# Performance work log

Measured on AMD Instinct MI355X. Metric: run time of the kernel, lower is better.

The kernel has to match this reference:

```python
import jax, jax.numpy as jnp
import numpy as np

B, S, N, D, H, C = 64, 4, 4096, 1024, 16, 14
HD = D // H
EPS = 1e-5


def _ln(x, g, b):
    m = jnp.mean(x, axis=-1, keepdims=True)
    v = jnp.mean((x - m) ** 2, axis=-1, keepdims=True)
    return (x - m) * jax.lax.rsqrt(v + EPS) * g + b


def setup_inputs() -> dict:
    key = jax.random.key(0)
    ks = jax.random.split(key, 12)
    std = 0.02
    return {
        "cls_tok": jax.random.normal(ks[0], (B, D), jnp.float32),
        "storage": jax.random.normal(ks[1], (B, S, D), jnp.float32),
        "patches": jax.random.normal(ks[2], (B, N, D), jnp.float32),
        "query": jax.random.normal(ks[3], (1, 1, D), jnp.float32) * std,
        "ln_kv_g": jnp.ones((D,), jnp.float32),
        "ln_kv_b": jnp.zeros((D,), jnp.float32),
        "Wq": jax.random.normal(ks[4], (D, D), jnp.float32) / np.sqrt(D).astype(np.float32),
        "Wk": jax.random.normal(ks[5], (D, D), jnp.float32) / np.sqrt(D).astype(np.float32),
        "Wv": jax.random.normal(ks[6], (D, D), jnp.float32) / np.sqrt(D).astype(np.float32),
        "bq": jnp.zeros((D,), jnp.float32),
        "bk": jnp.zeros((D,), jnp.float32),
        "bv": jnp.zeros((D,), jnp.float32),
        "Wo": jax.random.normal(ks[7], (D, D), jnp.float32) / np.sqrt(D).astype(np.float32),
        "bo": jnp.zeros((D,), jnp.float32),
        "ln_out_g": jnp.ones((D,), jnp.float32),
        "ln_out_b": jnp.zeros((D,), jnp.float32),
        "Wp": jax.random.normal(ks[8], (C, D), jnp.float32) * std,
        "bp": jnp.zeros((C,), jnp.float32),
    }


def reference(cls_tok, storage, patches, query, ln_kv_g, ln_kv_b,
              Wq, Wk, Wv, bq, bk, bv, Wo, bo, ln_out_g, ln_out_b, Wp, bp):
    # tokens: (B, L, D) with L = 1 + S + N
    tokens = jnp.concatenate([cls_tok[:, None, :], storage, patches], axis=1)
    kv = _ln(tokens, ln_kv_g, ln_kv_b)
    b = tokens.shape[0]
    q = jnp.broadcast_to(query, (b, 1, D))
    # torch MultiheadAttention: separate q/k/v projections then scaled dot-product
    qp = (q @ Wq.T + bq).reshape(b, 1, H, HD)
    kp = (kv @ Wk.T + bk).reshape(b, -1, H, HD)
    vp = (kv @ Wv.T + bv).reshape(b, -1, H, HD)
    scale = 1.0 / np.sqrt(HD).astype(np.float32)
    scores = jnp.einsum('bqhd,bkhd->bhqk', qp, kp) * scale  # (B, H, 1, L)
    attn = jax.nn.softmax(scores, axis=-1)
    ctx = jnp.einsum('bhqk,bkhd->bqhd', attn, vp).reshape(b, 1, D)
    pooled = ctx[:, 0] @ Wo.T + bo          # out projection, (B, D)
    pooled = _ln(pooled, ln_out_g, ln_out_b)
    return pooled @ Wp.T + bp               # (B, num_labels)
```

## Files before the change

### kernel.cpp

```cpp
#include <hip/hip_runtime.h>
#include <hip/hip_bf16.h>

#define BB 64
#define DD 1024
#define HH 16
#define LL 4101
#define NCH 8
#define CHUNK 513
#define SCALE 0.125f
#define LN_EPS 1e-5f
#define RGS 4104

typedef float  f32x4 __attribute__((ext_vector_type(4)));
typedef short  s16x8 __attribute__((ext_vector_type(8)));
typedef unsigned int u32x4 __attribute__((ext_vector_type(4)));

#define WS_QVEC 0
#define WS_GU   1024
#define WS_G    17408
#define WS_BU   17424
#define WS_CB   17440
#define WS_PL   17456
#define WS_PM   25648
#define WS_PA   33840
#define WS_CTX  8422448
#define WS_POOL 8487984

__device__ __forceinline__ unsigned int pk2(float a, float b) {
    __hip_bfloat162 h = __float22bfloat162_rn(make_float2(a, b));
    unsigned int r;
    __builtin_memcpy(&r, &h, 4);
    return r;
}

__device__ __forceinline__ const float* rowptr(int gr, int b, const float* cls,
                                               const float* sto, const float* pat) {
    if (gr == 0) return cls + (size_t)b * DD;
    if (gr <= 4) return sto + ((size_t)b * 4 + (gr - 1)) * DD;
    return pat + ((size_t)b * 4096 + (gr - 5)) * DD;
}

__global__ void k_qvec(const float* __restrict__ query, const float* __restrict__ Wq,
                       const float* __restrict__ bq, float* __restrict__ qvec) {
    int j = blockIdx.x; int lane = threadIdx.x;
    const float4* wr = reinterpret_cast<const float4*>(Wq + (size_t)j * DD);
    const float4* qr = reinterpret_cast<const float4*>(query);
    float s = 0.f;
#pragma unroll
    for (int k = 0; k < 4; ++k) {
        float4 a = wr[k * 64 + lane];
        float4 q = qr[k * 64 + lane];
        s += a.x * q.x + a.y * q.y + a.z * q.z + a.w * q.w;
    }
#pragma unroll
    for (int m = 1; m < 64; m <<= 1) s += __shfl_xor(s, m, 64);
    if (lane == 0) qvec[j] = s + bq[j];
}

__global__ void k_u(const float* __restrict__ Wk, const float* __restrict__ qvec,
                    const float* __restrict__ g, const float* __restrict__ bln,
                    float* __restrict__ gu, float* __restrict__ Gv, float* __restrict__ Bu) {
    int h = blockIdx.x; int tid = threadIdx.x;
    int w = tid >> 6, lane = tid & 63;
    __shared__ float qs[64];
    __shared__ float red[8];
    if (tid < 64) qs[tid] = qvec[h * 64 + tid];
    __syncthreads();
    int d0 = tid * 4;
    float ax = 0.f, ay = 0.f, az = 0.f, aw = 0.f;
    for (int i = 0; i < 64; ++i) {
        float q = qs[i];
        float4 wv = *reinterpret_cast<const float4*>(&Wk[(size_t)(h * 64 + i) * DD + d0]);
        ax += q * wv.x; ay += q * wv.y; az += q * wv.z; aw += q * wv.w;
    }
    float4 g4 = *reinterpret_cast<const float4*>(&g[d0]);
    float4 b4 = *reinterpret_cast<const float4*>(&bln[d0]);
    float ux = ax * SCALE, uy = ay * SCALE, uz = az * SCALE, uw = aw * SCALE;
    float4 gu4 = make_float4(ux * g4.x, uy * g4.y, uz * g4.z, uw * g4.w);
    *reinterpret_cast<float4*>(&gu[(size_t)h * DD + d0]) = gu4;
    float Gp = gu4.x + gu4.y + gu4.z + gu4.w;
    float Bp = ux * b4.x + uy * b4.y + uz * b4.z + uw * b4.w;
#pragma unroll
    for (int m = 1; m < 64; m <<= 1) { Gp += __shfl_xor(Gp, m, 64); Bp += __shfl_xor(Bp, m, 64); }
    if (lane == 0) { red[2 * w] = Gp; red[2 * w + 1] = Bp; }
    __syncthreads();
    if (tid == 0) {
        Gv[h] = red[0] + red[2] + red[4] + red[6];
        Bu[h] = red[1] + red[3] + red[5] + red[7];
    }
}

__global__ void k_cq(const float* __restrict__ qvec, const float* __restrict__ bk,
                     const float* __restrict__ Bu, float* __restrict__ CB) {
    int h = threadIdx.x;
    if (h < HH) {
        float s = 0.f;
        for (int i = 0; i < 64; ++i) s += qvec[h * 64 + i] * bk[h * 64 + i];
        CB[h] = Bu[h] + s * SCALE;
    }
}

__global__ __launch_bounds__(512, 4) void k_main(
    const float* __restrict__ cls, const float* __restrict__ sto,
    const float* __restrict__ pat, const float* __restrict__ gu,
    const float* __restrict__ Gv, const float* __restrict__ CBv,
    float* __restrict__ pA, float* __restrict__ pl, float* __restrict__ pM) {

    __shared__ __align__(16) ushort Xlds[8 * RGS];
    __shared__ __align__(16) f32x4 csr[8][64];
    __shared__ __align__(16) ushort alds[512];
    __shared__ float2 mrs[32];

    const int blk = blockIdx.x;
    const int b = blk >> 3, ch = blk & 7;
    const int row0 = ch * CHUNK;
    const int rows = min(CHUNK, LL - row0);
    const int nt = (rows + 31) >> 5;
    const int tid = threadIdx.x;
    const int w = tid >> 6, lane = tid & 63;
    const int lm = lane & 15, lg = lane >> 4;
    const int g = w >> 2, wk = w & 3;

    s16x8 guf[8];
    {
        const float* gubase = gu + (size_t)lm * DD + wk * 256 + lg * 8;
#pragma unroll
        for (int s = 0; s < 8; ++s) {
            const float* p = gubase + s * 32;
            u32x4 t;
#pragma unroll
            for (int j = 0; j < 4; ++j) t[j] = pk2(p[2 * j], p[2 * j + 1]);
            guf[s] = __builtin_bit_cast(s16x8, t);
        }
    }
    const float Gh = Gv[lm], CBh = CBv[lm];

    f32x4 acc[8];
#pragma unroll
    for (int i = 0; i < 8; ++i) acc[i] = (f32x4){0.f, 0.f, 0.f, 0.f};
    float lacc = 0.f, macc = 0.f;

    const int C0   = (g * 4 + (lm >> 2)) * RGS + wk * 1024 + (lg >> 1) * 64 + (lm & 3) * 16 + (lg & 1) * 8;
    const int bb4  = lg * 2 * RGS + w * 512 + lm;
    const int aoff = lm * 32 + lg * 8;

    for (int t = 0; t < nt; ++t) {
#pragma unroll
        for (int rr = 0; rr < 4; ++rr) {
            int rl = w * 4 + rr;
            int rloc = t * 32 + rl;
            bool valid = rloc < rows;
            float4 v[4];
#pragma unroll
            for (int it = 0; it < 4; ++it) v[it] = make_float4(0.f, 0.f, 0.f, 0.f);
            if (valid) {
                const float4* s4 = reinterpret_cast<const float4*>(
                    rowptr(row0 + rloc, b, cls, sto, pat));
#pragma unroll
                for (int it = 0; it < 4; ++it) v[it] = s4[it * 64 + lane];
            }
            float s1 = 0.f, s2 = 0.f;
#pragma unroll
            for (int it = 0; it < 4; ++it) {
                float4 q = v[it];
                s1 += q.x + q.y + q.z + q.w;
                s2 += q.x * q.x + q.y * q.y + q.z * q.z + q.w * q.w;
                uint2 pk;
                pk.x = pk2(q.x, q.y);
                pk.y = pk2(q.z, q.w);
                int d0 = 4 * (it * 64 + lane);
                int elem = (rl >> 2) * RGS + (d0 >> 4) * 64 + (rl & 3) * 16 + (d0 & 15);
                *reinterpret_cast<uint2*>(&Xlds[elem]) = pk;
            }
#pragma unroll
            for (int m = 1; m < 64; m <<= 1) {
                s1 += __shfl_xor(s1, m, 64);
                s2 += __shfl_xor(s2, m, 64);
            }
            if (lane == 0) {
                float mean = s1 * (1.f / 1024.f);
                float var = s2 * (1.f / 1024.f) - mean * mean;
                float rstd = rsqrtf(var + LN_EPS);
                mrs[rl] = make_float2(rstd, -mean * rstd);
            }
        }
        __syncthreads();

        {
            f32x4 c0 = {0.f, 0.f, 0.f, 0.f};
#pragma unroll
            for (int s = 0; s < 8; ++s) {
                s16x8 a0 = *reinterpret_cast<const s16x8*>(&Xlds[C0 + s * 128]);
                c0 = __builtin_amdgcn_mfma_f32_16x16x32_bf16(a0, guf[s], c0, 0, 0, 0);
            }
            csr[w][lane] = c0;
        }
        __syncthreads();

        {
#pragma unroll
            for (int gg = 0; gg < 2; ++gg) {
                f32x4 dv = csr[gg * 4][lane];
#pragma unroll
                for (int wp = 1; wp < 4; ++wp) dv += csr[gg * 4 + wp][lane];
                int rbase = gg * 16 + lg * 4;
                float al[4];
#pragma unroll
                for (int i = 0; i < 4; ++i) {
                    float2 mr = mrs[rbase + i];
                    float sc = dv[i] * mr.x + (mr.y * Gh + CBh);
                    bool vld = (t * 32 + rbase + i) < rows;
                    float p = vld ? __expf(sc) : 0.f;
                    lacc += p;
                    macc += p * mr.y;
                    al[i] = p * mr.x;
                }
                *reinterpret_cast<unsigned int*>(&alds[lm * 32 + rbase])     = pk2(al[0], al[1]);
                *reinterpret_cast<unsigned int*>(&alds[lm * 32 + rbase + 2]) = pk2(al[2], al[3]);
            }
        }
        asm volatile("s_waitcnt lgkmcnt(0)" ::: "memory");
        __builtin_amdgcn_sched_barrier(0);

        {
            s16x8 af = *reinterpret_cast<const s16x8*>(&alds[aoff]);
#pragma unroll
            for (int dt = 0; dt < 8; ++dt) {
                s16x8 bfrag;
#pragma unroll
                for (int j = 0; j < 8; ++j) {
                    int e = bb4 + dt * 64 + ((j & 3) << 4) + (j >> 2) * RGS;
                    bfrag[j] = (short)Xlds[e];
                }
                acc[dt] = __builtin_amdgcn_mfma_f32_16x16x32_bf16(af, bfrag, acc[dt], 0, 0, 0);
            }
        }
        __syncthreads();
    }

    size_t pabase = ((size_t)blk << 14);
#pragma unroll
    for (int dt = 0; dt < 8; ++dt) {
#pragma unroll
        for (int i = 0; i < 4; ++i) {
            int h = lg * 4 + i;
            pA[pabase + ((size_t)h << 10) + w * 128 + dt * 16 + lm] = acc[dt][i];
        }
    }
    if (w == 0) {
        lacc += __shfl_xor(lacc, 16, 64); lacc += __shfl_xor(lacc, 32, 64);
        macc += __shfl_xor(macc, 16, 64); macc += __shfl_xor(macc, 32, 64);
        if (lane < 16) {
            pl[blk * 16 + lane] = lacc;
            pM[blk * 16 + lane] = -macc;
        }
    }
}

__global__ void k_comb(float* __restrict__ pA, const float* __restrict__ pl,
                       const float* __restrict__ pM, const float* __restrict__ g,
                       const float* __restrict__ bln) {
    int blk = blockIdx.x; int b = blk >> 4; int h = blk & 15; int tid = threadIdx.x;
    float l = 0.f, M = 0.f;
#pragma unroll
    for (int ch = 0; ch < NCH; ++ch) {
        l += pl[(b * NCH + ch) * 16 + h];
        M += pM[(b * NCH + ch) * 16 + h];
    }
    float inv = 1.f / l;
    float4 s = make_float4(0.f, 0.f, 0.f, 0.f);
#pragma unroll
    for (int ch = 0; ch < NCH; ++ch) {
        const float4* p4 = reinterpret_cast<const float4*>(
            pA + (((size_t)(b * NCH + ch) * 16 + h) << 10));
        float4 v = p4[tid];
        s.x += v.x; s.y += v.y; s.z += v.z; s.w += v.w;
    }
    float4 g4 = *reinterpret_cast<const float4*>(&g[tid * 4]);
    float4 b4 = *reinterpret_cast<const float4*>(&bln[tid * 4]);
    float4 o;
    o.x = g4.x * (s.x - M) * inv + b4.x;
    o.y = g4.y * (s.y - M) * inv + b4.y;
    o.z = g4.z * (s.z - M) * inv + b4.z;
    o.w = g4.w * (s.w - M) * inv + b4.w;
    float4* dst = reinterpret_cast<float4*>(pA + (((size_t)(b * NCH) * 16 + h) << 10));
    dst[tid] = o;
}

__global__ void k_ctx(const float* __restrict__ Wv, const float* __restrict__ bv,
                      const float* __restrict__ pA, float* __restrict__ ctx) {
    int j = blockIdx.x; int h = j >> 6;
    int w = threadIdx.x >> 6, lane = threadIdx.x & 63;
    const float4* wr = reinterpret_cast<const float4*>(Wv + (size_t)j * DD);
    float4 wv[4];
#pragma unroll
    for (int k = 0; k < 4; ++k) wv[k] = wr[k * 64 + lane];
    float bvj = bv[j];
    for (int bb2 = w * 16; bb2 < w * 16 + 16; ++bb2) {
        const float4* sr = reinterpret_cast<const float4*>(
            pA + (((size_t)(bb2 * NCH) * 16 + h) << 10));
        float s = 0.f;
#pragma unroll
        for (int k = 0; k < 4; ++k) {
            float4 v = sr[k * 64 + lane];
            s += wv[k].x * v.x + wv[k].y * v.y + wv[k].z * v.z + wv[k].w * v.w;
        }
#pragma unroll
        for (int m = 1; m < 64; m <<= 1) s += __shfl_xor(s, m, 64);
        if (lane == 0) ctx[(size_t)bb2 * DD + j] = s + bvj;
    }
}

__global__ void k_pool(const float* __restrict__ Wo, const float* __restrict__ bo,
                       const float* __restrict__ ctx, float* __restrict__ pooled) {
    int j = blockIdx.x;
    int w = threadIdx.x >> 6, lane = threadIdx.x & 63;
    const float4* wr = reinterpret_cast<const float4*>(Wo + (size_t)j * DD);
    float4 wv[4];
#pragma unroll
    for (int k = 0; k < 4; ++k) wv[k] = wr[k * 64 + lane];
    float boj = bo[j];
    for (int bb2 = w * 16; bb2 < w * 16 + 16; ++bb2) {
        const float4* cr4 = reinterpret_cast<const float4*>(ctx + (size_t)bb2 * DD);
        float s = 0.f;
#pragma unroll
        for (int k = 0; k < 4; ++k) {
            float4 v = cr4[k * 64 + lane];
            s += wv[k].x * v.x + wv[k].y * v.y + wv[k].z * v.z + wv[k].w * v.w;
        }
#pragma unroll
        for (int m = 1; m < 64; m <<= 1) s += __shfl_xor(s, m, 64);
        if (lane == 0) pooled[(size_t)bb2 * DD + j] = s + boj;
    }
}

__global__ void k_head(const float* __restrict__ pooled, const float* __restrict__ g2,
                       const float* __restrict__ b2, const float* __restrict__ Wp,
                       const float* __restrict__ bp, float* __restrict__ out) {
    int b = blockIdx.x; int tid = threadIdx.x;
    __shared__ float pln[DD];
    __shared__ float red[8];
    const float4* pr = reinterpret_cast<const float4*>(pooled + (size_t)b * DD);
    float4 v = pr[tid];
    float s1 = v.x + v.y + v.z + v.w;
    float s2 = v.x * v.x + v.y * v.y + v.z * v.z + v.w * v.w;
#pragma unroll
    for (int m = 1; m < 64; m <<= 1) { s1 += __shfl_xor(s1, m, 64); s2 += __shfl_xor(s2, m, 64); }
    int w = tid >> 6, lane = tid & 63;
    if (lane == 0) { red[2 * w] = s1; red[2 * w + 1] = s2; }
    __syncthreads();
    s1 = red[0] + red[2] + red[4] + red[6];
    s2 = red[1] + red[3] + red[5] + red[7];
    float mean = s1 * (1.f / 1024.f);
    float var  = s2 * (1.f / 1024.f) - mean * mean;
    float rstd = rsqrtf(var + LN_EPS);
    int d0 = tid * 4;
    pln[d0 + 0] = (v.x - mean) * rstd * g2[d0 + 0] + b2[d0 + 0];
    pln[d0 + 1] = (v.y - mean) * rstd * g2[d0 + 1] + b2[d0 + 1];
    pln[d0 + 2] = (v.z - mean) * rstd * g2[d0 + 2] + b2[d0 + 2];
    pln[d0 + 3] = (v.w - mean) * rstd * g2[d0 + 3] + b2[d0 + 3];
    __syncthreads();
    int q = tid & 15, c = tid >> 4;
    if (c < 14) {
        float s = 0.f;
#pragma unroll 8
        for (int i = 0; i < 64; ++i) {
            int d = i * 16 + q;
            s += pln[d] * Wp[c * DD + d];
        }
#pragma unroll
        for (int m = 1; m < 16; m <<= 1) s += __shfl_xor(s, m, 64);
        if (q == 0) out[b * 14 + c] = s + bp[c];
    }
}

extern "C" void kernel_launch(void* const* d_in, const int* in_sizes, int n_in,
                              void* d_out, int out_size, void* d_ws, size_t ws_size,
                              hipStream_t stream) {
    const float* cls   = (const float*)d_in[0];
    const float* sto   = (const float*)d_in[1];
    const float* pat   = (const float*)d_in[2];
    const float* query = (const float*)d_in[3];
    const float* g     = (const float*)d_in[4];
    const float* bln   = (const float*)d_in[5];
    const float* Wq    = (const float*)d_in[6];
    const float* Wk    = (const float*)d_in[7];
    const float* Wv    = (const float*)d_in[8];
    const float* bq    = (const float*)d_in[9];
    const float* bk    = (const float*)d_in[10];
    const float* bv    = (const float*)d_in[11];
    const float* Wo    = (const float*)d_in[12];
    const float* bo    = (const float*)d_in[13];
    const float* g2    = (const float*)d_in[14];
    const float* b2    = (const float*)d_in[15];
    const float* Wp    = (const float*)d_in[16];
    const float* bp    = (const float*)d_in[17];

    float* ws     = (float*)d_ws;
    float* qvec   = ws + WS_QVEC;
    float* gu     = ws + WS_GU;
    float* Gv     = ws + WS_G;
    float* Bu     = ws + WS_BU;
    float* CB     = ws + WS_CB;
    float* pl     = ws + WS_PL;
    float* pM     = ws + WS_PM;
    float* pA     = ws + WS_PA;
    float* ctx    = ws + WS_CTX;
    float* pooled = ws + WS_POOL;
    float* out    = (float*)d_out;

    hipLaunchKernelGGL(k_qvec, dim3(1024), dim3(64), 0, stream, query, Wq, bq, qvec);
    hipLaunchKernelGGL(k_u,    dim3(16),   dim3(256), 0, stream, Wk, qvec, g, bln, gu, Gv, Bu);
    hipLaunchKernelGGL(k_cq,   dim3(1),    dim3(64), 0, stream, qvec, bk, Bu, CB);
    hipLaunchKernelGGL(k_main, dim3(BB * NCH), dim3(512), 0, stream,
                       cls, sto, pat, gu, Gv, CB, pA, pl, pM);
    hipLaunchKernelGGL(k_comb, dim3(BB * HH), dim3(256), 0, stream, pA, pl, pM, g, bln);
    hipLaunchKernelGGL(k_ctx,  dim3(1024), dim3(256), 0, stream, Wv, bv, pA, ctx);
    hipLaunchKernelGGL(k_pool, dim3(1024), dim3(256), 0, stream, Wo, bo, ctx, pooled);
    hipLaunchKernelGGL(k_head, dim3(64),   dim3(256), 0, stream, pooled, g2, b2, Wp, bp, out);
}
```

Before: 287.3 us.

## Double-buffer 16-row LDS tiles and prefetch next rows into registers

Shrinks the per-iteration tile from 32 to 16 rows and keeps two LDS buffers in a simple row-major layout with padded row stride. The next tile's global rows are prefetched into registers while the current tile is processed, and the score MFMA reduction is split across all 8 waves. The value-accumulation MFMA runs once per pair of tiles, drawing its K=32 operand from both buffers. It also swaps __syncthreads for explicit waitcnt plus s_barrier. The aim is to hide global load latency behind compute and cut LDS footprint for occupancy, at the cost of more loop iterations and barriers, plus extra register pressure from the prefetch buffer.

```diff
diff --git a/kernel.cpp b/kernel.cpp
--- a/kernel.cpp
+++ b/kernel.cpp
@@ -9,7 +9,8 @@
 #define CHUNK 513
 #define SCALE 0.125f
 #define LN_EPS 1e-5f
-#define RGS 4104
+#define XROW 1032
+#define XBUF (16 * XROW)
 
 typedef float  f32x4 __attribute__((ext_vector_type(4)));
 typedef short  s16x8 __attribute__((ext_vector_type(8)));
@@ -106,26 +107,25 @@
     const float* __restrict__ Gv, const float* __restrict__ CBv,
     float* __restrict__ pA, float* __restrict__ pl, float* __restrict__ pM) {
 
-    __shared__ __align__(16) ushort Xlds[8 * RGS];
+    __shared__ __align__(16) ushort Xb[2 * XBUF];
     __shared__ __align__(16) f32x4 csr[8][64];
-    __shared__ __align__(16) ushort alds[512];
-    __shared__ float2 mrs[32];
+    __shared__ __align__(16) ushort alds[16 * 32];
+    __shared__ float2 mrs[16];
 
     const int blk = blockIdx.x;
     const int b = blk >> 3, ch = blk & 7;
     const int row0 = ch * CHUNK;
     const int rows = min(CHUNK, LL - row0);
-    const int nt = (rows + 31) >> 5;
+    const int nt = (rows + 15) >> 4;
     const int tid = threadIdx.x;
     const int w = tid >> 6, lane = tid & 63;
     const int lm = lane & 15, lg = lane >> 4;
-    const int g = w >> 2, wk = w & 3;
-
-    s16x8 guf[8];
+
+    s16x8 guf[4];
     {
-        const float* gubase = gu + (size_t)lm * DD + wk * 256 + lg * 8;
-#pragma unroll
-        for (int s = 0; s < 8; ++s) {
+        const float* gubase = gu + (size_t)lm * DD + w * 128 + lg * 8;
+#pragma unroll
+        for (int s = 0; s < 4; ++s) {
             const float* p = gubase + s * 32;
             u32x4 t;
 #pragma unroll
@@ -140,37 +140,39 @@
     for (int i = 0; i < 8; ++i) acc[i] = (f32x4){0.f, 0.f, 0.f, 0.f};
     float lacc = 0.f, macc = 0.f;
 
-    const int C0   = (g * 4 + (lm >> 2)) * RGS + wk * 1024 + (lg >> 1) * 64 + (lm & 3) * 16 + (lg & 1) * 8;
-    const int bb4  = lg * 2 * RGS + w * 512 + lm;
+    const int C0   = lm * XROW + w * 128 + lg * 8;
     const int aoff = lm * 32 + lg * 8;
 
+    float4 pf[2][4];
+#pragma unroll
+    for (int rr = 0; rr < 2; ++rr) {
+#pragma unroll
+        for (int it = 0; it < 4; ++it) pf[rr][it] = make_float4(0.f, 0.f, 0.f, 0.f);
+        int rloc = 2 * w + rr;
+        if (rloc < rows) {
+            const float4* s4 = reinterpret_cast<const float4*>(
+                rowptr(row0 + rloc, b, cls, sto, pat));
+#pragma unroll
+            for (int it = 0; it < 4; ++it) pf[rr][it] = s4[it * 64 + lane];
+        }
+    }
+
+    int cur = 0;
     for (int t = 0; t < nt; ++t) {
 #pragma unroll
-        for (int rr = 0; rr < 4; ++rr) {
-            int rl = w * 4 + rr;
-            int rloc = t * 32 + rl;
-            bool valid = rloc < rows;
-            float4 v[4];
-#pragma unroll
-            for (int it = 0; it < 4; ++it) v[it] = make_float4(0.f, 0.f, 0.f, 0.f);
-            if (valid) {
-                const float4* s4 = reinterpret_cast<const float4*>(
-                    rowptr(row0 + rloc, b, cls, sto, pat));
-#pragma unroll
-                for (int it = 0; it < 4; ++it) v[it] = s4[it * 64 + lane];
-            }
+        for (int rr = 0; rr < 2; ++rr) {
+            int rl = 2 * w + rr;
             float s1 = 0.f, s2 = 0.f;
 #pragma unroll
             for (int it = 0; it < 4; ++it) {
-                float4 q = v[it];
+                float4 q = pf[rr][it];
                 s1 += q.x + q.y + q.z + q.w;
                 s2 += q.x * q.x + q.y * q.y + q.z * q.z + q.w * q.w;
                 uint2 pk;
                 pk.x = pk2(q.x, q.y);
                 pk.y = pk2(q.z, q.w);
-                int d0 = 4 * (it * 64 + lane);
-                int elem = (rl >> 2) * RGS + (d0 >> 4) * 64 + (rl & 3) * 16 + (d0 & 15);
-                *reinterpret_cast<uint2*>(&Xlds[elem]) = pk;
+                int e = cur * XBUF + rl * XROW + it * 256 + lane * 4;
+                *reinterpret_cast<uint2*>(&Xb[e]) = pk;
             }
 #pragma unroll
             for (int m = 1; m < 64; m <<= 1) {
@@ -184,58 +186,80 @@
                 mrs[rl] = make_float2(rstd, -mean * rstd);
             }
         }
-        __syncthreads();
+#pragma unroll
+        for (int rr = 0; rr < 2; ++rr) {
+#pragma unroll
+            for (int it = 0; it < 4; ++it) pf[rr][it] = make_float4(0.f, 0.f, 0.f, 0.f);
+            int rloc = (t + 1) * 16 + 2 * w + rr;
+            if (t + 1 < nt && rloc < rows) {
+                const float4* s4 = reinterpret_cast<const float4*>(
+                    rowptr(row0 + rloc, b, cls, sto, pat));
+#pragma unroll
+                for (int it = 0; it < 4; ++it) pf[rr][it] = s4[it * 64 + lane];
+            }
+        }
+        asm volatile("s_waitcnt lgkmcnt(0)" ::: "memory");
+        __builtin_amdgcn_s_barrier();
 
         {
             f32x4 c0 = {0.f, 0.f, 0.f, 0.f};
 #pragma unroll
-            for (int s = 0; s < 8; ++s) {
-                s16x8 a0 = *reinterpret_cast<const s16x8*>(&Xlds[C0 + s * 128]);
+            for (int s = 0; s < 4; ++s) {
+                s16x8 a0 = *reinterpret_cast<const s16x8*>(&Xb[cur * XBUF + C0 + s * 32]);
                 c0 = __builtin_amdgcn_mfma_f32_16x16x32_bf16(a0, guf[s], c0, 0, 0, 0);
             }
             csr[w][lane] = c0;
         }
-        __syncthreads();
+        asm volatile("s_waitcnt lgkmcnt(0)" ::: "memory");
+        __builtin_amdgcn_s_barrier();
 
         {
-#pragma unroll
-            for (int gg = 0; gg < 2; ++gg) {
-                f32x4 dv = csr[gg * 4][lane];
-#pragma unroll
-                for (int wp = 1; wp < 4; ++wp) dv += csr[gg * 4 + wp][lane];
-                int rbase = gg * 16 + lg * 4;
-                float al[4];
-#pragma unroll
-                for (int i = 0; i < 4; ++i) {
-                    float2 mr = mrs[rbase + i];
-                    float sc = dv[i] * mr.x + (mr.y * Gh + CBh);
-                    bool vld = (t * 32 + rbase + i) < rows;
-                    float p = vld ? __expf(sc) : 0.f;
-                    lacc += p;
-                    macc += p * mr.y;
-                    al[i] = p * mr.x;
-                }
-                *reinterpret_cast<unsigned int*>(&alds[lm * 32 + rbase])     = pk2(al[0], al[1]);
-                *reinterpret_cast<unsigned int*>(&alds[lm * 32 + rbase + 2]) = pk2(al[2], al[3]);
+            f32x4 dv = csr[0][lane];
+#pragma unroll
+            for (int wp = 1; wp < 8; ++wp) dv += csr[wp][lane];
+            int rbase = lg * 4;
+            int p16 = (t & 1) * 16;
+            float al[4];
+#pragma unroll
+            for (int i = 0; i < 4; ++i) {
+                float2 mr = mrs[rbase + i];
+                float sc = dv[i] * mr.x + (mr.y * Gh + CBh);
+                bool vld = (t * 16 + rbase + i) < rows;
+                float p = vld ? __expf(sc) : 0.f;
+                lacc += p;
+                macc += p * mr.y;
+                al[i] = p * mr.x;
+            }
+            *reinterpret_cast<unsigned int*>(&alds[lm * 32 + p16 + rbase])     = pk2(al[0], al[1]);
+            *reinterpret_cast<unsigned int*>(&alds[lm * 32 + p16 + rbase + 2]) = pk2(al[2], al[3]);
+            if ((t == nt - 1) && !(t & 1)) {
+                *reinterpret_cast<unsigned int*>(&alds[lm * 32 + 16 + rbase])     = 0u;
+                *reinterpret_cast<unsigned int*>(&alds[lm * 32 + 16 + rbase + 2]) = 0u;
             }
         }
         asm volatile("s_waitcnt lgkmcnt(0)" ::: "memory");
         __builtin_amdgcn_sched_barrier(0);
 
-        {
+        if ((t & 1) || (t == nt - 1)) {
+            int bufA = (t & 1) ? (cur ^ 1) : cur;
+            int bufB = cur;
+            int myBuf = (lg >= 2) ? bufB : bufA;
+            int rbase16 = (lg * 8) & 15;
+            const ushort* xb = &Xb[myBuf * XBUF + rbase16 * XROW + w * 128 + lm];
             s16x8 af = *reinterpret_cast<const s16x8*>(&alds[aoff]);
 #pragma unroll
             for (int dt = 0; dt < 8; ++dt) {
                 s16x8 bfrag;
 #pragma unroll
                 for (int j = 0; j < 8; ++j) {
-                    int e = bb4 + dt * 64 + ((j & 3) << 4) + (j >> 2) * RGS;
-                    bfrag[j] = (short)Xlds[e];
+                    bfrag[j] = (short)xb[dt * 16 + j * XROW];
                 }
                 acc[dt] = __builtin_amdgcn_mfma_f32_16x16x32_bf16(af, bfrag, acc[dt], 0, 0, 0);
             }
         }
-        __syncthreads();
+        asm volatile("s_waitcnt lgkmcnt(0)" ::: "memory");
+        __builtin_amdgcn_s_barrier();
+        cur ^= 1;
     }
 
     size_t pabase = ((size_t)blk << 14);
```

Result: slower. 353.6 us (+23.1%).

## Double-buffer row tiles via async global-to-LDS loads and MFMA-based LN stats

Applied to the files above, without the earlier changes.

The main kernel now streams 16-row fp32 tiles straight into a double-buffered LDS region with global_load_lds, so the next tile's loads overlap compute on the current one. Per-row LayerNorm sums are computed with extra MFMAs (x·x and x·ones) instead of shuffle reductions, and the chunk count drops from 8 to 4 per batch with one block per CU. The u-vector precompute is also split across 4x more blocks, with partial sums combined in k_cq. This trades grid parallelism (256 blocks) and bf16 conversion done during LDS reads for overlapped memory traffic.

```diff
diff --git a/kernel.cpp b/kernel.cpp
--- a/kernel.cpp
+++ b/kernel.cpp
@@ -5,11 +5,12 @@
 #define DD 1024
 #define HH 16
 #define LL 4101
-#define NCH 8
-#define CHUNK 513
+#define NCH 4
+#define CHUNK 1026
 #define SCALE 0.125f
 #define LN_EPS 1e-5f
-#define RGS 4104
+#define XROWF 1028
+#define BUFF  (16 * XROWF)
 
 typedef float  f32x4 __attribute__((ext_vector_type(4)));
 typedef short  s16x8 __attribute__((ext_vector_type(8)));
@@ -18,13 +19,14 @@
 #define WS_QVEC 0
 #define WS_GU   1024
 #define WS_G    17408
-#define WS_BU   17424
-#define WS_CB   17440
-#define WS_PL   17456
-#define WS_PM   25648
-#define WS_PA   33840
-#define WS_CTX  8422448
-#define WS_POOL 8487984
+#define WS_CB   17424
+#define WS_GP   17440
+#define WS_BP   17504
+#define WS_PL   17568
+#define WS_PM   21664
+#define WS_PA   25760
+#define WS_CTX  4220064
+#define WS_POOL 4285600
 
 __device__ __forceinline__ unsigned int pk2(float a, float b) {
     __hip_bfloat162 h = __float22bfloat162_rn(make_float2(a, b));
@@ -59,80 +61,86 @@
 
 __global__ void k_u(const float* __restrict__ Wk, const float* __restrict__ qvec,
                     const float* __restrict__ g, const float* __restrict__ bln,
-                    float* __restrict__ gu, float* __restrict__ Gv, float* __restrict__ Bu) {
-    int h = blockIdx.x; int tid = threadIdx.x;
+                    float* __restrict__ gu, float* __restrict__ Gp, float* __restrict__ Bp) {
+    int h = blockIdx.x >> 2, q = blockIdx.x & 3;
+    int tid = threadIdx.x;
     int w = tid >> 6, lane = tid & 63;
     __shared__ float qs[64];
     __shared__ float red[8];
     if (tid < 64) qs[tid] = qvec[h * 64 + tid];
     __syncthreads();
-    int d0 = tid * 4;
-    float ax = 0.f, ay = 0.f, az = 0.f, aw = 0.f;
-    for (int i = 0; i < 64; ++i) {
-        float q = qs[i];
-        float4 wv = *reinterpret_cast<const float4*>(&Wk[(size_t)(h * 64 + i) * DD + d0]);
-        ax += q * wv.x; ay += q * wv.y; az += q * wv.z; aw += q * wv.w;
-    }
-    float4 g4 = *reinterpret_cast<const float4*>(&g[d0]);
-    float4 b4 = *reinterpret_cast<const float4*>(&bln[d0]);
-    float ux = ax * SCALE, uy = ay * SCALE, uz = az * SCALE, uw = aw * SCALE;
-    float4 gu4 = make_float4(ux * g4.x, uy * g4.y, uz * g4.z, uw * g4.w);
-    *reinterpret_cast<float4*>(&gu[(size_t)h * DD + d0]) = gu4;
-    float Gp = gu4.x + gu4.y + gu4.z + gu4.w;
-    float Bp = ux * b4.x + uy * b4.y + uz * b4.z + uw * b4.w;
-#pragma unroll
-    for (int m = 1; m < 64; m <<= 1) { Gp += __shfl_xor(Gp, m, 64); Bp += __shfl_xor(Bp, m, 64); }
-    if (lane == 0) { red[2 * w] = Gp; red[2 * w + 1] = Bp; }
+    int d = q * 256 + tid;
+    float a = 0.f;
+#pragma unroll 8
+    for (int i = 0; i < 64; ++i) a += qs[i] * Wk[(size_t)(h * 64 + i) * DD + d];
+    float u = a * SCALE;
+    float guv = u * g[d];
+    gu[(size_t)h * DD + d] = guv;
+    float Gv_ = guv, Bv_ = u * bln[d];
+#pragma unroll
+    for (int m = 1; m < 64; m <<= 1) { Gv_ += __shfl_xor(Gv_, m, 64); Bv_ += __shfl_xor(Bv_, m, 64); }
+    if (lane == 0) { red[2 * w] = Gv_; red[2 * w + 1] = Bv_; }
     __syncthreads();
     if (tid == 0) {
-        Gv[h] = red[0] + red[2] + red[4] + red[6];
-        Bu[h] = red[1] + red[3] + red[5] + red[7];
+        Gp[h * 4 + q] = red[0] + red[2] + red[4] + red[6];
+        Bp[h * 4 + q] = red[1] + red[3] + red[5] + red[7];
     }
 }
 
 __global__ void k_cq(const float* __restrict__ qvec, const float* __restrict__ bk,
-                     const float* __restrict__ Bu, float* __restrict__ CB) {
+                     const float* __restrict__ Gp, const float* __restrict__ Bp,
+                     float* __restrict__ Gv, float* __restrict__ CB) {
     int h = threadIdx.x;
     if (h < HH) {
+        float G = Gp[h * 4] + Gp[h * 4 + 1] + Gp[h * 4 + 2] + Gp[h * 4 + 3];
+        float Bu = Bp[h * 4] + Bp[h * 4 + 1] + Bp[h * 4 + 2] + Bp[h * 4 + 3];
         float s = 0.f;
         for (int i = 0; i < 64; ++i) s += qvec[h * 64 + i] * bk[h * 64 + i];
-        CB[h] = Bu[h] + s * SCALE;
-    }
-}
-
-__global__ __launch_bounds__(512, 4) void k_main(
+        Gv[h] = G;
+        CB[h] = Bu + s * SCALE;
+    }
+}
+
+__global__ __launch_bounds__(512, 1) void k_main(
     const float* __restrict__ cls, const float* __restrict__ sto,
     const float* __restrict__ pat, const float* __restrict__ gu,
     const float* __restrict__ Gv, const float* __restrict__ CBv,
     float* __restrict__ pA, float* __restrict__ pl, float* __restrict__ pM) {
 
-    __shared__ __align__(16) ushort Xlds[8 * RGS];
+    __shared__ __align__(16) float Xf[2 * BUFF];
     __shared__ __align__(16) f32x4 csr[8][64];
-    __shared__ __align__(16) ushort alds[512];
-    __shared__ float2 mrs[32];
+    __shared__ float sstat[2][16][8];
+    __shared__ float2 mrs[16];
+    __shared__ __align__(8) ushort alds[16 * 32];
 
     const int blk = blockIdx.x;
-    const int b = blk >> 3, ch = blk & 7;
+    const int b = blk >> 2, ch = blk & 3;
     const int row0 = ch * CHUNK;
     const int rows = min(CHUNK, LL - row0);
-    const int nt = (rows + 31) >> 5;
+    const int nt = (rows + 15) >> 4;
     const int tid = threadIdx.x;
     const int w = tid >> 6, lane = tid & 63;
     const int lm = lane & 15, lg = lane >> 4;
-    const int g = w >> 2, wk = w & 3;
-
-    s16x8 guf[8];
+
+    for (int i = tid; i < 2 * BUFF; i += 512) Xf[i] = 0.f;
+    if (tid < 256) reinterpret_cast<unsigned int*>(alds)[tid] = 0u;
+
+    s16x8 guf[4];
     {
-        const float* gubase = gu + (size_t)lm * DD + wk * 256 + lg * 8;
-#pragma unroll
-        for (int s = 0; s < 8; ++s) {
+        const float* gubase = gu + (size_t)lm * DD + w * 128 + lg * 8;
+#pragma unroll
+        for (int s = 0; s < 4; ++s) {
             const float* p = gubase + s * 32;
             u32x4 t;
 #pragma unroll
             for (int j = 0; j < 4; ++j) t[j] = pk2(p[2 * j], p[2 * j + 1]);
-            guf[s] = __builtin_bit_cast(s16x8, t);
-        }
-    }
+            s16x8 f; __builtin_memcpy(&f, &t, 16);
+            guf[s] = f;
+        }
+    }
+    s16x8 ones;
+#pragma unroll
+    for (int j = 0; j < 8; ++j) ones[j] = (short)0x3F80;
     const float Gh = Gv[lm], CBh = CBv[lm];
 
     f32x4 acc[8];
@@ -140,102 +148,116 @@
     for (int i = 0; i < 8; ++i) acc[i] = (f32x4){0.f, 0.f, 0.f, 0.f};
     float lacc = 0.f, macc = 0.f;
 
-    const int C0   = (g * 4 + (lm >> 2)) * RGS + wk * 1024 + (lg >> 1) * 64 + (lm & 3) * 16 + (lg & 1) * 8;
-    const int bb4  = lg * 2 * RGS + w * 512 + lm;
-    const int aoff = lm * 32 + lg * 8;
+#define ISSUE_TILE(T)                                                              \
+    {                                                                              \
+        int buf_ = (T) & 1;                                                        \
+        _Pragma("unroll")                                                          \
+        for (int rr = 0; rr < 2; ++rr) {                                           \
+            int rl = 2 * w + rr;                                                   \
+            int rloc = (T) * 16 + rl;                                              \
+            if (rloc < rows) {                                                     \
+                const float* rp = rowptr(row0 + rloc, b, cls, sto, pat);           \
+                _Pragma("unroll")                                                  \
+                for (int c = 0; c < 4; ++c) {                                      \
+                    __builtin_amdgcn_global_load_lds(                              \
+                        (const __attribute__((address_space(1))) unsigned int*)    \
+                            (rp + c * 256 + lane * 4),                             \
+                        (__attribute__((address_space(3))) unsigned int*)          \
+                            (&Xf[buf_ * BUFF + rl * XROWF + c * 256]),             \
+                        16, 0, 0);                                                 \
+                }                                                                  \
+            }                                                                      \
+        }                                                                          \
+    }
+
+    __syncthreads();
+    ISSUE_TILE(0);
+    __syncthreads();
 
     for (int t = 0; t < nt; ++t) {
-#pragma unroll
-        for (int rr = 0; rr < 4; ++rr) {
-            int rl = w * 4 + rr;
-            int rloc = t * 32 + rl;
-            bool valid = rloc < rows;
-            float4 v[4];
-#pragma unroll
-            for (int it = 0; it < 4; ++it) v[it] = make_float4(0.f, 0.f, 0.f, 0.f);
-            if (valid) {
-                const float4* s4 = reinterpret_cast<const float4*>(
-                    rowptr(row0 + rloc, b, cls, sto, pat));
-#pragma unroll
-                for (int it = 0; it < 4; ++it) v[it] = s4[it * 64 + lane];
-            }
-            float s1 = 0.f, s2 = 0.f;
-#pragma unroll
-            for (int it = 0; it < 4; ++it) {
-                float4 q = v[it];
-                s1 += q.x + q.y + q.z + q.w;
-                s2 += q.x * q.x + q.y * q.y + q.z * q.z + q.w * q.w;
-                uint2 pk;
-                pk.x = pk2(q.x, q.y);
-                pk.y = pk2(q.z, q.w);
-                int d0 = 4 * (it * 64 + lane);
-                int elem = (rl >> 2) * RGS + (d0 >> 4) * 64 + (rl & 3) * 16 + (d0 & 15);
-                *reinterpret_cast<uint2*>(&Xlds[elem]) = pk;
-            }
-#pragma unroll
-            for (int m = 1; m < 64; m <<= 1) {
-                s1 += __shfl_xor(s1, m, 64);
-                s2 += __shfl_xor(s2, m, 64);
-            }
-            if (lane == 0) {
-                float mean = s1 * (1.f / 1024.f);
-                float var = s2 * (1.f / 1024.f) - mean * mean;
-                float rstd = rsqrtf(var + LN_EPS);
-                mrs[rl] = make_float2(rstd, -mean * rstd);
-            }
-        }
-        __syncthreads();
+        const int buf = t & 1;
+        if (t + 1 < nt) ISSUE_TILE(t + 1);
 
         {
-            f32x4 c0 = {0.f, 0.f, 0.f, 0.f};
-#pragma unroll
-            for (int s = 0; s < 8; ++s) {
-                s16x8 a0 = *reinterpret_cast<const s16x8*>(&Xlds[C0 + s * 128]);
+            f32x4 c0 = {0.f,0.f,0.f,0.f}, q0 = {0.f,0.f,0.f,0.f}, m0 = {0.f,0.f,0.f,0.f};
+            const float* Ab = &Xf[buf * BUFF + lm * XROWF + w * 128 + lg * 8];
+#pragma unroll
+            for (int s = 0; s < 4; ++s) {
+                float4 x0 = *reinterpret_cast<const float4*>(Ab + s * 32);
+                float4 x1 = *reinterpret_cast<const float4*>(Ab + s * 32 + 4);
+                u32x4 tt;
+                tt[0] = pk2(x0.x, x0.y); tt[1] = pk2(x0.z, x0.w);
+                tt[2] = pk2(x1.x, x1.y); tt[3] = pk2(x1.z, x1.w);
+                s16x8 a0; __builtin_memcpy(&a0, &tt, 16);
                 c0 = __builtin_amdgcn_mfma_f32_16x16x32_bf16(a0, guf[s], c0, 0, 0, 0);
+                q0 = __builtin_amdgcn_mfma_f32_16x16x32_bf16(a0, a0,     q0, 0, 0, 0);
+                m0 = __builtin_amdgcn_mfma_f32_16x16x32_bf16(a0, ones,   m0, 0, 0, 0);
             }
             csr[w][lane] = c0;
-        }
-        __syncthreads();
-
-        {
-#pragma unroll
-            for (int gg = 0; gg < 2; ++gg) {
-                f32x4 dv = csr[gg * 4][lane];
-#pragma unroll
-                for (int wp = 1; wp < 4; ++wp) dv += csr[gg * 4 + wp][lane];
-                int rbase = gg * 16 + lg * 4;
-                float al[4];
-#pragma unroll
-                for (int i = 0; i < 4; ++i) {
-                    float2 mr = mrs[rbase + i];
-                    float sc = dv[i] * mr.x + (mr.y * Gh + CBh);
-                    bool vld = (t * 32 + rbase + i) < rows;
-                    float p = vld ? __expf(sc) : 0.f;
-                    lacc += p;
-                    macc += p * mr.y;
-                    al[i] = p * mr.x;
-                }
-                *reinterpret_cast<unsigned int*>(&alds[lm * 32 + rbase])     = pk2(al[0], al[1]);
-                *reinterpret_cast<unsigned int*>(&alds[lm * 32 + rbase + 2]) = pk2(al[2], al[3]);
+            if (lg == (lm >> 2)) sstat[0][lm][w] = q0[lm & 3];
+            if (lm == 0) {
+#pragma unroll
+                for (int i = 0; i < 4; ++i) sstat[1][lg * 4 + i][w] = m0[i];
             }
+        }
+        asm volatile("s_waitcnt lgkmcnt(0)" ::: "memory");
+        __builtin_amdgcn_s_barrier();
+
+        if (lane < 16) {
+            const float4* q4 = reinterpret_cast<const float4*>(&sstat[0][lane][0]);
+            float4 qa = q4[0], qb = q4[1];
+            const float4* m4 = reinterpret_cast<const float4*>(&sstat[1][lane][0]);
+            float4 ma = m4[0], mb = m4[1];
+            float s2 = qa.x + qa.y + qa.z + qa.w + qb.x + qb.y + qb.z + qb.w;
+            float s1 = ma.x + ma.y + ma.z + ma.w + mb.x + mb.y + mb.z + mb.w;
+            float mean = s1 * (1.f / 1024.f);
+            float var  = s2 * (1.f / 1024.f) - mean * mean;
+            float rstd = rsqrtf(var + LN_EPS);
+            mrs[lane] = make_float2(rstd, -mean * rstd);
         }
         asm volatile("s_waitcnt lgkmcnt(0)" ::: "memory");
         __builtin_amdgcn_sched_barrier(0);
-
         {
-            s16x8 af = *reinterpret_cast<const s16x8*>(&alds[aoff]);
+            f32x4 dv = csr[0][lane];
+#pragma unroll
+            for (int wp = 1; wp < 8; ++wp) dv += csr[wp][lane];
+            int rbase = lg * 4;
+            float al[4];
+#pragma unroll
+            for (int i = 0; i < 4; ++i) {
+                float2 mr = mrs[rbase + i];
+                float sc = dv[i] * mr.x + (mr.y * Gh + CBh);
+                bool vld = (t * 16 + rbase + i) < rows;
+                float p = vld ? __expf(sc) : 0.f;
+                lacc += p;
+                macc += p * mr.y;
+                al[i] = p * mr.x;
+            }
+            *reinterpret_cast<unsigned int*>(&alds[lm * 32 + rbase])     = pk2(al[0], al[1]);
+            *reinterpret_cast<unsigned int*>(&alds[lm * 32 + rbase + 2]) = pk2(al[2], al[3]);
+        }
+        asm volatile("s_waitcnt lgkmcnt(0)" ::: "memory");
+        __builtin_amdgcn_sched_barrier(0);
+
+        {
+            s16x8 af = *reinterpret_cast<const s16x8*>(&alds[lm * 32 + lg * 8]);
+            const float* Bb = &Xf[buf * BUFF + (lg & 1) * 8 * XROWF + w * 128 + lm];
+            bool act = lg < 2;
 #pragma unroll
             for (int dt = 0; dt < 8; ++dt) {
-                s16x8 bfrag;
-#pragma unroll
-                for (int j = 0; j < 8; ++j) {
-                    int e = bb4 + dt * 64 + ((j & 3) << 4) + (j >> 2) * RGS;
-                    bfrag[j] = (short)Xlds[e];
-                }
-                acc[dt] = __builtin_amdgcn_mfma_f32_16x16x32_bf16(af, bfrag, acc[dt], 0, 0, 0);
+                float bx[8];
+#pragma unroll
+                for (int j = 0; j < 8; ++j) bx[j] = act ? Bb[j * XROWF + dt * 16] : 0.f;
+                u32x4 tb;
+                tb[0] = pk2(bx[0], bx[1]); tb[1] = pk2(bx[2], bx[3]);
+                tb[2] = pk2(bx[4], bx[5]); tb[3] = pk2(bx[6], bx[7]);
+                s16x8 bf; __builtin_memcpy(&bf, &tb, 16);
+                acc[dt] = __builtin_amdgcn_mfma_f32_16x16x32_bf16(af, bf, acc[dt], 0, 0, 0);
             }
         }
-        __syncthreads();
+        asm volatile("s_waitcnt vmcnt(0)" ::: "memory");
+        asm volatile("s_waitcnt lgkmcnt(0)" ::: "memory");
+        __builtin_amdgcn_s_barrier();
     }
 
     size_t pabase = ((size_t)blk << 14);
@@ -255,6 +277,7 @@
             pM[blk * 16 + lane] = -macc;
         }
     }
+#undef ISSUE_TILE
 }
 
 __global__ void k_comb(float* __restrict__ pA, const float* __restrict__ pl,
@@ -400,8 +423,9 @@
     float* qvec   = ws + WS_QVEC;
     float* gu     = ws + WS_GU;
     float* Gv     = ws + WS_G;
-    float* Bu     = ws + WS_BU;
     float* CB     = ws + WS_CB;
+    float* Gp     = ws + WS_GP;
+    float* Bp     = ws + WS_BP;
     float* pl     = ws + WS_PL;
     float* pM     = ws + WS_PM;
     float* pA     = ws + WS_PA;
@@ -410,8 +434,8 @@
     float* out    = (float*)d_out;
 
     hipLaunchKernelGGL(k_qvec, dim3(1024), dim3(64), 0, stream, query, Wq, bq, qvec);
-    hipLaunchKernelGGL(k_u,    dim3(16),   dim3(256), 0, stream, Wk, qvec, g, bln, gu, Gv, Bu);
-    hipLaunchKernelGGL(k_cq,   dim3(1),    dim3(64), 0, stream, qvec, bk, Bu, CB);
+    hipLaunchKernelGGL(k_u,    dim3(64),   dim3(256), 0, stream, Wk, qvec, g, bln, gu, Gp, Bp);
+    hipLaunchKernelGGL(k_cq,   dim3(1),    dim3(64), 0, stream, qvec, bk, Gp, Bp, Gv, CB);
     hipLaunchKernelGGL(k_main, dim3(BB * NCH), dim3(512), 0, stream,
                        cls, sto, pat, gu, Gv, CB, pA, pl, pM);
     hipLaunchKernelGGL(k_comb, dim3(BB * HH), dim3(256), 0, stream, pA, pl, pM, g, bln);
```

Result: slower. 428.4 us (+49.1%).

## Shrink main attention blocks to 4 waves and split sequence into 12 chunks

Applied to the files above, without the earlier changes.

The main fused LN+score+weighted-sum kernel now uses 256-thread blocks processing 16 rows per tile instead of 512 threads and 32 rows. Each wave owns a full 256-wide slice of the D dimension with 16 accumulators. The sequence is split into 12 chunks when workspace permits, giving more blocks for better occupancy and CU coverage. The k_u precompute is also spread over 64 blocks with partial sums reduced in k_cq. The trade-offs are more partial results to combine, half-idle lanes in the weighted-sum MFMA, and more register pressure from the larger accumulator set.

```diff
diff --git a/kernel.cpp b/kernel.cpp
--- a/kernel.cpp
+++ b/kernel.cpp
@@ -5,11 +5,9 @@
 #define DD 1024
 #define HH 16
 #define LL 4101
-#define NCH 8
-#define CHUNK 513
 #define SCALE 0.125f
 #define LN_EPS 1e-5f
-#define RGS 4104
+#define RGS 4112
 
 typedef float  f32x4 __attribute__((ext_vector_type(4)));
 typedef short  s16x8 __attribute__((ext_vector_type(8)));
@@ -18,13 +16,12 @@
 #define WS_QVEC 0
 #define WS_GU   1024
 #define WS_G    17408
-#define WS_BU   17424
-#define WS_CB   17440
-#define WS_PL   17456
-#define WS_PM   25648
-#define WS_PA   33840
-#define WS_CTX  8422448
-#define WS_POOL 8487984
+#define WS_CB   17424
+#define WS_GP   17440
+#define WS_BP   17504
+#define WS_PL   17568
+#define WS_PM   29856
+#define WS_PA   42144
 
 __device__ __forceinline__ unsigned int pk2(float a, float b) {
     __hip_bfloat162 h = __float22bfloat162_rn(make_float2(a, b));
@@ -59,96 +56,99 @@
 
 __global__ void k_u(const float* __restrict__ Wk, const float* __restrict__ qvec,
                     const float* __restrict__ g, const float* __restrict__ bln,
-                    float* __restrict__ gu, float* __restrict__ Gv, float* __restrict__ Bu) {
-    int h = blockIdx.x; int tid = threadIdx.x;
+                    float* __restrict__ gu, float* __restrict__ Gp, float* __restrict__ Bp) {
+    int h = blockIdx.x >> 2, q = blockIdx.x & 3;
+    int tid = threadIdx.x;
     int w = tid >> 6, lane = tid & 63;
     __shared__ float qs[64];
     __shared__ float red[8];
     if (tid < 64) qs[tid] = qvec[h * 64 + tid];
     __syncthreads();
-    int d0 = tid * 4;
-    float ax = 0.f, ay = 0.f, az = 0.f, aw = 0.f;
-    for (int i = 0; i < 64; ++i) {
-        float q = qs[i];
-        float4 wv = *reinterpret_cast<const float4*>(&Wk[(size_t)(h * 64 + i) * DD + d0]);
-        ax += q * wv.x; ay += q * wv.y; az += q * wv.z; aw += q * wv.w;
-    }
-    float4 g4 = *reinterpret_cast<const float4*>(&g[d0]);
-    float4 b4 = *reinterpret_cast<const float4*>(&bln[d0]);
-    float ux = ax * SCALE, uy = ay * SCALE, uz = az * SCALE, uw = aw * SCALE;
-    float4 gu4 = make_float4(ux * g4.x, uy * g4.y, uz * g4.z, uw * g4.w);
-    *reinterpret_cast<float4*>(&gu[(size_t)h * DD + d0]) = gu4;
-    float Gp = gu4.x + gu4.y + gu4.z + gu4.w;
-    float Bp = ux * b4.x + uy * b4.y + uz * b4.z + uw * b4.w;
-#pragma unroll
-    for (int m = 1; m < 64; m <<= 1) { Gp += __shfl_xor(Gp, m, 64); Bp += __shfl_xor(Bp, m, 64); }
-    if (lane == 0) { red[2 * w] = Gp; red[2 * w + 1] = Bp; }
+    int d = q * 256 + tid;
+    float a = 0.f;
+#pragma unroll 8
+    for (int i = 0; i < 64; ++i) a += qs[i] * Wk[(size_t)(h * 64 + i) * DD + d];
+    float u = a * SCALE;
+    float guv = u * g[d];
+    gu[(size_t)h * DD + d] = guv;
+    float Gv_ = guv, Bv_ = u * bln[d];
+#pragma unroll
+    for (int m = 1; m < 64; m <<= 1) { Gv_ += __shfl_xor(Gv_, m, 64); Bv_ += __shfl_xor(Bv_, m, 64); }
+    if (lane == 0) { red[2 * w] = Gv_; red[2 * w + 1] = Bv_; }
     __syncthreads();
     if (tid == 0) {
-        Gv[h] = red[0] + red[2] + red[4] + red[6];
-        Bu[h] = red[1] + red[3] + red[5] + red[7];
+        Gp[h * 4 + q] = red[0] + red[2] + red[4] + red[6];
+        Bp[h * 4 + q] = red[1] + red[3] + red[5] + red[7];
     }
 }
 
 __global__ void k_cq(const float* __restrict__ qvec, const float* __restrict__ bk,
-                     const float* __restrict__ Bu, float* __restrict__ CB) {
+                     const float* __restrict__ Gp, const float* __restrict__ Bp,
+                     float* __restrict__ Gv, float* __restrict__ CB) {
     int h = threadIdx.x;
     if (h < HH) {
+        float G = Gp[h * 4] + Gp[h * 4 + 1] + Gp[h * 4 + 2] + Gp[h * 4 + 3];
+        float Bu = Bp[h * 4] + Bp[h * 4 + 1] + Bp[h * 4 + 2] + Bp[h * 4 + 3];
         float s = 0.f;
         for (int i = 0; i < 64; ++i) s += qvec[h * 64 + i] * bk[h * 64 + i];
-        CB[h] = Bu[h] + s * SCALE;
-    }
-}
-
-__global__ __launch_bounds__(512, 4) void k_main(
+        Gv[h] = G;
+        CB[h] = Bu + s * SCALE;
+    }
+}
+
+__global__ __launch_bounds__(256, 3) void k_main(
     const float* __restrict__ cls, const float* __restrict__ sto,
     const float* __restrict__ pat, const float* __restrict__ gu,
     const float* __restrict__ Gv, const float* __restrict__ CBv,
-    float* __restrict__ pA, float* __restrict__ pl, float* __restrict__ pM) {
-
-    __shared__ __align__(16) ushort Xlds[8 * RGS];
-    __shared__ __align__(16) f32x4 csr[8][64];
-    __shared__ __align__(16) ushort alds[512];
-    __shared__ float2 mrs[32];
+    float* __restrict__ pA, float* __restrict__ pl, float* __restrict__ pM,
+    int nch, int chunk) {
+
+    __shared__ __align__(16) ushort Xs[4 * RGS];
+    __shared__ __align__(16) f32x4 csr[4][64];
+    __shared__ __align__(8) ushort alds[512];
+    __shared__ float2 mrs[16];
 
     const int blk = blockIdx.x;
-    const int b = blk >> 3, ch = blk & 7;
-    const int row0 = ch * CHUNK;
-    const int rows = min(CHUNK, LL - row0);
-    const int nt = (rows + 31) >> 5;
+    const int b = blk / nch, ch = blk - b * nch;
+    const int row0 = ch * chunk;
+    const int rows = min(chunk, LL - row0);
+    const int nt = (rows + 15) >> 4;
     const int tid = threadIdx.x;
     const int w = tid >> 6, lane = tid & 63;
     const int lm = lane & 15, lg = lane >> 4;
-    const int g = w >> 2, wk = w & 3;
+
+    if (tid < 256) reinterpret_cast<unsigned int*>(alds)[tid] = 0u;
 
     s16x8 guf[8];
     {
-        const float* gubase = gu + (size_t)lm * DD + wk * 256 + lg * 8;
+        const float* gubase = gu + (size_t)lm * DD + w * 256 + lg * 8;
 #pragma unroll
         for (int s = 0; s < 8; ++s) {
             const float* p = gubase + s * 32;
             u32x4 t;
 #pragma unroll
             for (int j = 0; j < 4; ++j) t[j] = pk2(p[2 * j], p[2 * j + 1]);
-            guf[s] = __builtin_bit_cast(s16x8, t);
+            s16x8 f; __builtin_memcpy(&f, &t, 16);
+            guf[s] = f;
         }
     }
     const float Gh = Gv[lm], CBh = CBv[lm];
 
-    f32x4 acc[8];
-#pragma unroll
-    for (int i = 0; i < 8; ++i) acc[i] = (f32x4){0.f, 0.f, 0.f, 0.f};
+    f32x4 acc[16];
+#pragma unroll
+    for (int i = 0; i < 16; ++i) acc[i] = (f32x4){0.f, 0.f, 0.f, 0.f};
     float lacc = 0.f, macc = 0.f;
 
-    const int C0   = (g * 4 + (lm >> 2)) * RGS + wk * 1024 + (lg >> 1) * 64 + (lm & 3) * 16 + (lg & 1) * 8;
-    const int bb4  = lg * 2 * RGS + w * 512 + lm;
-    const int aoff = lm * 32 + lg * 8;
+    const int C0 = (lm >> 2) * RGS + w * 1024 + (lg >> 1) * 64 + (lm & 3) * 16 + (lg & 1) * 8;
+    const bool act = lg < 2;
+
+    __syncthreads();
 
     for (int t = 0; t < nt; ++t) {
-#pragma unroll
+#pragma unroll 2
         for (int rr = 0; rr < 4; ++rr) {
             int rl = w * 4 + rr;
-            int rloc = t * 32 + rl;
+            int rloc = t * 16 + rl;
             bool valid = rloc < rows;
             float4 v[4];
 #pragma unroll
@@ -170,7 +170,7 @@
                 pk.y = pk2(q.z, q.w);
                 int d0 = 4 * (it * 64 + lane);
                 int elem = (rl >> 2) * RGS + (d0 >> 4) * 64 + (rl & 3) * 16 + (d0 & 15);
-                *reinterpret_cast<uint2*>(&Xlds[elem]) = pk;
+                *reinterpret_cast<uint2*>(&Xs[elem]) = pk;
             }
 #pragma unroll
             for (int m = 1; m < 64; m <<= 1) {
@@ -190,7 +190,7 @@
             f32x4 c0 = {0.f, 0.f, 0.f, 0.f};
 #pragma unroll
             for (int s = 0; s < 8; ++s) {
-                s16x8 a0 = *reinterpret_cast<const s16x8*>(&Xlds[C0 + s * 128]);
+                s16x8 a0 = *reinterpret_cast<const s16x8*>(&Xs[C0 + s * 128]);
                 c0 = __builtin_amdgcn_mfma_f32_16x16x32_bf16(a0, guf[s], c0, 0, 0, 0);
             }
             csr[w][lane] = c0;
@@ -198,39 +198,36 @@
         __syncthreads();
 
         {
-#pragma unroll
-            for (int gg = 0; gg < 2; ++gg) {
-                f32x4 dv = csr[gg * 4][lane];
-#pragma unroll
-                for (int wp = 1; wp < 4; ++wp) dv += csr[gg * 4 + wp][lane];
-                int rbase = gg * 16 + lg * 4;
-                float al[4];
-#pragma unroll
-                for (int i = 0; i < 4; ++i) {
-                    float2 mr = mrs[rbase + i];
-                    float sc = dv[i] * mr.x + (mr.y * Gh + CBh);
-                    bool vld = (t * 32 + rbase + i) < rows;
-                    float p = vld ? __expf(sc) : 0.f;
-                    lacc += p;
-                    macc += p * mr.y;
-                    al[i] = p * mr.x;
-                }
-                *reinterpret_cast<unsigned int*>(&alds[lm * 32 + rbase])     = pk2(al[0], al[1]);
-                *reinterpret_cast<unsigned int*>(&alds[lm * 32 + rbase + 2]) = pk2(al[2], al[3]);
-            }
+            f32x4 dv = csr[0][lane];
+#pragma unroll
+            for (int wp = 1; wp < 4; ++wp) dv += csr[wp][lane];
+            int rbase = lg * 4;
+            float al[4];
+#pragma unroll
+            for (int i = 0; i < 4; ++i) {
+                float2 mr = mrs[rbase + i];
+                float sc = dv[i] * mr.x + (mr.y * Gh + CBh);
+                bool vld = (t * 16 + rbase + i) < rows;
+                float p = vld ? __expf(sc) : 0.f;
+                lacc += p;
+                macc += p * mr.y;
+                al[i] = p * mr.x;
+            }
+            *reinterpret_cast<unsigned int*>(&alds[lm * 32 + rbase])     = pk2(al[0], al[1]);
+            *reinterpret_cast<unsigned int*>(&alds[lm * 32 + rbase + 2]) = pk2(al[2], al[3]);
         }
         asm volatile("s_waitcnt lgkmcnt(0)" ::: "memory");
         __builtin_amdgcn_sched_barrier(0);
 
         {
-            s16x8 af = *reinterpret_cast<const s16x8*>(&alds[aoff]);
-#pragma unroll
-            for (int dt = 0; dt < 8; ++dt) {
+            s16x8 af = *reinterpret_cast<const s16x8*>(&alds[lm * 32 + lg * 8]);
+#pragma unroll
+            for (int dt = 0; dt < 16; ++dt) {
                 s16x8 bfrag;
 #pragma unroll
                 for (int j = 0; j < 8; ++j) {
-                    int e = bb4 + dt * 64 + ((j & 3) << 4) + (j >> 2) * RGS;
-                    bfrag[j] = (short)Xlds[e];
+                    int e = (lg * 2 + (j >> 2)) * RGS + (w * 16 + dt) * 64 + (j & 3) * 16 + lm;
+                    bfrag[j] = act ? (short)Xs[e] : (short)0;
                 }
                 acc[dt] = __builtin_amdgcn_mfma_f32_16x16x32_bf16(af, bfrag, acc[dt], 0, 0, 0);
             }
@@ -240,11 +237,11 @@
 
     size_t pabase = ((size_t)blk << 14);
 #pragma unroll
-    for (int dt = 0; dt < 8; ++dt) {
+    for (int dt = 0; dt < 16; ++dt) {
 #pragma unroll
         for (int i = 0; i < 4; ++i) {
             int h = lg * 4 + i;
-            pA[pabase + ((size_t)h << 10) + w * 128 + dt * 16 + lm] = acc[dt][i];
+            pA[pabase + ((size_t)h << 10) + w * 256 + dt * 16 + lm] = acc[dt][i];
         }
     }
     if (w == 0) {
@@ -259,20 +256,18 @@
 
 __global__ void k_comb(float* __restrict__ pA, const float* __restrict__ pl,
                        const float* __restrict__ pM, const float* __restrict__ g,
-                       const float* __restrict__ bln) {
+                       const float* __restrict__ bln, int nch) {
     int blk = blockIdx.x; int b = blk >> 4; int h = blk & 15; int tid = threadIdx.x;
     float l = 0.f, M = 0.f;
-#pragma unroll
-    for (int ch = 0; ch < NCH; ++ch) {
-        l += pl[(b * NCH + ch) * 16 + h];
-        M += pM[(b * NCH + ch) * 16 + h];
+    for (int ch = 0; ch < nch; ++ch) {
+        l += pl[(b * nch + ch) * 16 + h];
+        M += pM[(b * nch + ch) * 16 + h];
     }
     float inv = 1.f / l;
     float4 s = make_float4(0.f, 0.f, 0.f, 0.f);
-#pragma unroll
-    for (int ch = 0; ch < NCH; ++ch) {
+    for (int ch = 0; ch < nch; ++ch) {
         const float4* p4 = reinterpret_cast<const float4*>(
-            pA + (((size_t)(b * NCH + ch) * 16 + h) << 10));
+            pA + (((size_t)(b * nch + ch) * 16 + h) << 10));
         float4 v = p4[tid];
         s.x += v.x; s.y += v.y; s.z += v.z; s.w += v.w;
     }
@@ -283,12 +278,12 @@
     o.y = g4.y * (s.y - M) * inv + b4.y;
     o.z = g4.z * (s.z - M) * inv + b4.z;
     o.w = g4.w * (s.w - M) * inv + b4.w;
-    float4* dst = reinterpret_cast<float4*>(pA + (((size_t)(b * NCH) * 16 + h) << 10));
+    float4* dst = reinterpret_cast<float4*>(pA + (((size_t)(b * nch) * 16 + h) << 10));
     dst[tid] = o;
 }
 
 __global__ void k_ctx(const float* __restrict__ Wv, const float* __restrict__ bv,
-                      const float* __restrict__ pA, float* __restrict__ ctx) {
+                      const float* __restrict__ pA, float* __restrict__ ctx, int nch) {
     int j = blockIdx.x; int h = j >> 6;
     int w = threadIdx.x >> 6, lane = threadIdx.x & 63;
     const float4* wr = reinterpret_cast<const float4*>(Wv + (size_t)j * DD);
@@ -298,7 +293,7 @@
     float bvj = bv[j];
     for (int bb2 = w * 16; bb2 < w * 16 + 16; ++bb2) {
         const float4* sr = reinterpret_cast<const float4*>(
-            pA + (((size_t)(bb2 * NCH) * 16 + h) << 10));
+            pA + (((size_t)(bb2 * nch) * 16 + h) << 10));
         float s = 0.f;
 #pragma unroll
         for (int k = 0; k < 4; ++k) {
@@ -396,26 +391,31 @@
     const float* Wp    = (const float*)d_in[16];
     const float* bp    = (const float*)d_in[17];
 
+    size_t need12 = ((size_t)WS_PA + (size_t)64 * 12 * 16 * 1024 + 2 * 65536) * 4;
+    int nch = (ws_size >= need12) ? 12 : 8;
+    int chunk = (LL + nch - 1) / nch;
+
     float* ws     = (float*)d_ws;
     float* qvec   = ws + WS_QVEC;
     float* gu     = ws + WS_GU;
     float* Gv     = ws + WS_G;
-    float* Bu     = ws + WS_BU;
     float* CB     = ws + WS_CB;
+    float* Gp     = ws + WS_GP;
+    float* Bp     = ws + WS_BP;
     float* pl     = ws + WS_PL;
     float* pM     = ws + WS_PM;
     float* pA     = ws + WS_PA;
-    float* ctx    = ws + WS_CTX;
-    float* pooled = ws + WS_POOL;
+    float* ctx    = pA + (size_t)64 * nch * 16 * 1024;
+    float* pooled = ctx + 65536;
     float* out    = (float*)d_out;
 
     hipLaunchKernelGGL(k_qvec, dim3(1024), dim3(64), 0, stream, query, Wq, bq, qvec);
-    hipLaunchKernelGGL(k_u,    dim3(16),   dim3(256), 0, stream, Wk, qvec, g, bln, gu, Gv, Bu);
-    hipLaunchKernelGGL(k_cq,   dim3(1),    dim3(64), 0, stream, qvec, bk, Bu, CB);
-    hipLaunchKernelGGL(k_main, dim3(BB * NCH), dim3(512), 0, stream,
-                       cls, sto, pat, gu, Gv, CB, pA, pl, pM);
-    hipLaunchKernelGGL(k_comb, dim3(BB * HH), dim3(256), 0, stream, pA, pl, pM, g, bln);
-    hipLaunchKernelGGL(k_ctx,  dim3(1024), dim3(256), 0, stream, Wv, bv, pA, ctx);
+    hipLaunchKernelGGL(k_u,    dim3(64),   dim3(256), 0, stream, Wk, qvec, g, bln, gu, Gp, Bp);
+    hipLaunchKernelGGL(k_cq,   dim3(1),    dim3(64), 0, stream, qvec, bk, Gp, Bp, Gv, CB);
+    hipLaunchKernelGGL(k_main, dim3(BB * nch), dim3(256), 0, stream,
+                       cls, sto, pat, gu, Gv, CB, pA, pl, pM, nch, chunk);
+    hipLaunchKernelGGL(k_comb, dim3(BB * HH), dim3(256), 0, stream, pA, pl, pM, g, bln, nch);
+    hipLaunchKernelGGL(k_ctx,  dim3(1024), dim3(256), 0, stream, Wv, bv, pA, ctx, nch);
     hipLaunchKernelGGL(k_pool, dim3(1024), dim3(256), 0, stream, Wo, bo, ctx, pooled);
     hipLaunchKernelGGL(k_head, dim3(64),   dim3(256), 0, stream, pooled, g2, b2, Wp, bp, out);
 }
```

Measured after the change: 284.5 us. No clear change (-0.9%).
